# Optimization experiments

Hardware: AMD Instinct MI355X
Metric: run time of the kernel (lower is better)

Reference implementation:

```python
import jax, jax.numpy as jnp
import numpy as np

N_NODES = 50000
N_EDGES = 800000
HID = 128
HEADS = 1
VOCAB = 1001  # input_dim + 1
OUT = 16
NEG_SLOPE = 0.2  # DGL GATv2Conv default


def setup_inputs():
    key = jax.random.key(0)
    ks = jax.random.split(key, 12)
    s = 1.0 / np.sqrt(HID)
    inp = {}
    inp['feats'] = jax.random.randint(ks[0], (N_NODES, 2), 0, VOCAB, dtype=jnp.int64)
    inp['src'] = jax.random.randint(ks[1], (N_EDGES,), 0, N_NODES, dtype=jnp.int32)
    inp['dst'] = jax.random.randint(ks[2], (N_EDGES,), 0, N_NODES, dtype=jnp.int32)
    inp['key_emb'] = jax.random.normal(ks[3], (VOCAB, HID), jnp.float32)
    inp['val_emb'] = jax.random.normal(ks[4], (VOCAB, HID), jnp.float32)
    inp['W1'] = jax.random.uniform(ks[5], (HID, HEADS * HID), jnp.float32, -s, s)
    inp['attn1'] = jax.random.uniform(ks[6], (HEADS, HID), jnp.float32, -s, s)
    inp['W2'] = jax.random.uniform(ks[7], (HID, HEADS * HID), jnp.float32, -s, s)
    inp['attn2'] = jax.random.uniform(ks[8], (HEADS, HID), jnp.float32, -s, s)
    inp['cls_w'] = jax.random.uniform(ks[9], (HID, OUT), jnp.float32, -s, s)
    return inp


def _gatv2_layer(h, W, attn, src, dst):
    # share_weights=True: one linear transform for both src and dst roles
    feat = (h @ W).reshape(N_NODES, HEADS, HID)          # [N,H,D]
    e = jax.nn.leaky_relu(feat[src] + feat[dst], NEG_SLOPE)  # [E,H,D]
    logits = jnp.einsum('ehd,hd->eh', e, attn)            # [E,H]
    # segment softmax over incoming edges of each dst node
    m = jax.ops.segment_max(logits, dst, num_segments=N_NODES)  # [N,H]
    ex = jnp.exp(logits - m[dst])
    denom = jax.ops.segment_sum(ex, dst, num_segments=N_NODES)
    a = ex / denom[dst]                                   # [E,H]
    # weighted scatter-aggregate of src features to dst nodes
    return jax.ops.segment_sum(a[:, :, None] * feat[src], dst, num_segments=N_NODES)  # [N,H,D]


def reference(feats, src, dst, key_emb, val_emb, W1, attn1, W2, attn2, cls_w):
    h = jax.nn.relu(key_emb[feats[:, 0]] + val_emb[feats[:, 1]])  # [N,HID]
    h = _gatv2_layer(h, W1, attn1, src, dst).mean(axis=1)         # mean over heads
    h = _gatv2_layer(h, W2, attn2, src, dst).mean(axis=1)
    return h @ cls_w  # [N,OUT]
```

## Files before the change

### kernel.cpp

```cpp
#include <hip/hip_runtime.h>
#include <hip/hip_fp16.h>
#include <math.h>

#define HID 128

typedef _Float16 half8 __attribute__((ext_vector_type(8)));
typedef float floatx4 __attribute__((ext_vector_type(4)));

struct h4pack { __half2 a, b; };

__device__ __forceinline__ float4 h4tof4(h4pack h) {
  float2 lo = __half22float2(h.a);
  float2 hi = __half22float2(h.b);
  return make_float4(lo.x, lo.y, hi.x, hi.y);
}

__device__ __forceinline__ h4pack f4toh4(float4 v) {
  h4pack h;
  h.a = __floats2half2_rn(v.x, v.y);
  h.b = __floats2half2_rn(v.z, v.w);
  return h;
}

__global__ __launch_bounds__(256) void zero_kernel(int4* __restrict__ p, int n4) {
  int i = blockIdx.x * 256 + threadIdx.x;
  if (i < n4) p[i] = make_int4(0, 0, 0, 0);
}

__global__ __launch_bounds__(256) void hist_kernel(
    const int* __restrict__ dst, int* __restrict__ counts,
    int* __restrict__ rank, int E) {
  int e = blockIdx.x * 256 + threadIdx.x;
  if (e < E) rank[e] = atomicAdd(&counts[dst[e]], 1);
}

__global__ __launch_bounds__(256) void partial_kernel(
    const int* __restrict__ counts, int* __restrict__ partials, int N) {
  __shared__ int s[256];
  int idx = blockIdx.x * 256 + threadIdx.x;
  int c = (idx < N) ? counts[idx] : 0;
  s[threadIdx.x] = (idx < N) ? ((c + 7) & ~7) : 0;
  __syncthreads();
  for (int o = 128; o > 0; o >>= 1) {
    if (threadIdx.x < o) s[threadIdx.x] += s[threadIdx.x + o];
    __syncthreads();
  }
  if (threadIdx.x == 0) partials[blockIdx.x] = s[0];
}

__global__ __launch_bounds__(256) void scan2_kernel(
    const int* __restrict__ partials, int* __restrict__ bases, int NB) {
  __shared__ int s[256];
  int t = threadIdx.x;
  int v0 = (t < NB) ? partials[t] : 0;
  s[t] = v0;
  __syncthreads();
  for (int o = 1; o < 256; o <<= 1) {
    int v = (t >= o) ? s[t - o] : 0;
    __syncthreads();
    s[t] += v;
    __syncthreads();
  }
  bases[t] = s[t] - v0;
}

__global__ __launch_bounds__(256) void offs_kernel(
    const int* __restrict__ counts, const int* __restrict__ bases,
    int* __restrict__ offs, int* __restrict__ csr, int N) {
  __shared__ int s[256];
  int t = threadIdx.x;
  int idx = blockIdx.x * 256 + t;
  int deg = (idx < N) ? counts[idx] : 0;
  int c = (idx < N) ? ((deg + 7) & ~7) : 0;
  s[t] = c;
  __syncthreads();
  for (int o = 1; o < 256; o <<= 1) {
    int v = (t >= o) ? s[t - o] : 0;
    __syncthreads();
    s[t] += v;
    __syncthreads();
  }
  int base = bases[blockIdx.x];
  if (idx < N) {
    int o = base + s[t] - c;
    offs[idx] = o;
    for (int k = deg; k < c; ++k) csr[o + k] = 0;
  }
  if (idx == N - 1) offs[N] = base + s[t];
}

__global__ __launch_bounds__(256) void scatter_kernel(
    const int* __restrict__ src, const int* __restrict__ dst,
    const int* __restrict__ offs, const int* __restrict__ rank,
    int* __restrict__ csr, int E) {
  int e = blockIdx.x * 256 + threadIdx.x;
  if (e >= E) return;
  csr[offs[dst[e]] + rank[e]] = src[e];
}

__global__ __launch_bounds__(256) void embed_kernel(
    const int* __restrict__ feats, const float* __restrict__ ke,
    const float* __restrict__ ve, __half* __restrict__ h0, int N) {
  int gid = blockIdx.x * 256 + threadIdx.x;
  int n = gid >> 4, j = gid & 15;
  if (n >= N) return;
  int f0 = feats[2 * n], f1 = feats[2 * n + 1];
  const float4* a4 = (const float4*)(ke + (size_t)f0 * HID) + j * 2;
  const float4* b4 = (const float4*)(ve + (size_t)f1 * HID) + j * 2;
  float4 a0 = a4[0], a1 = a4[1], b0 = b4[0], b1 = b4[1];
  float4 v0, v1;
  v0.x = fmaxf(a0.x + b0.x, 0.f); v0.y = fmaxf(a0.y + b0.y, 0.f);
  v0.z = fmaxf(a0.z + b0.z, 0.f); v0.w = fmaxf(a0.w + b0.w, 0.f);
  v1.x = fmaxf(a1.x + b1.x, 0.f); v1.y = fmaxf(a1.y + b1.y, 0.f);
  v1.z = fmaxf(a1.z + b1.z, 0.f); v1.w = fmaxf(a1.w + b1.w, 0.f);
  h4pack* out = (h4pack*)h0 + (size_t)n * 32 + j * 2;
  out[0] = f4toh4(v0);
  out[1] = f4toh4(v1);
}

__global__ __launch_bounds__(256) void wprep_kernel(
    const float* __restrict__ W, __half* __restrict__ Wt) {
  int t = blockIdx.x * 256 + threadIdx.x;
  int k = t >> 7, c = t & 127;
  Wt[(size_t)c * HID + k] = __float2half(W[t]);
}

__global__ __launch_bounds__(256) void gemm_mfma_kernel(
    const __half* __restrict__ A, const __half* __restrict__ Wt,
    __half* __restrict__ F, int N) {
  int w = threadIdx.x >> 6;
  int lane = threadIdx.x & 63;
  int r = lane & 15, g = lane >> 4;
  int row0 = blockIdx.x * 64 + w * 16;
  if (row0 >= N) return;
  int arow = row0 + r;
  if (arow >= N) arow = N - 1;
  const half8* Ap = (const half8*)(A + (size_t)arow * HID + g * 8);
  half8 a0 = Ap[0];
  half8 a1 = Ap[4];
  half8 a2 = Ap[8];
  half8 a3 = Ap[12];
#pragma unroll
  for (int ct = 0; ct < 8; ++ct) {
    const half8* Bp = (const half8*)(Wt + (size_t)(ct * 16 + r) * HID + g * 8);
    half8 b0 = Bp[0], b1 = Bp[4], b2 = Bp[8], b3 = Bp[12];
    floatx4 c = {0.f, 0.f, 0.f, 0.f};
    c = __builtin_amdgcn_mfma_f32_16x16x32_f16(a0, b0, c, 0, 0, 0);
    c = __builtin_amdgcn_mfma_f32_16x16x32_f16(a1, b1, c, 0, 0, 0);
    c = __builtin_amdgcn_mfma_f32_16x16x32_f16(a2, b2, c, 0, 0, 0);
    c = __builtin_amdgcn_mfma_f32_16x16x32_f16(a3, b3, c, 0, 0, 0);
    int col = ct * 16 + r;
#pragma unroll
    for (int reg = 0; reg < 4; ++reg) {
      int row = row0 + g * 4 + reg;
      if (row < N) F[(size_t)row * HID + col] = __float2half(c[reg]);
    }
  }
}

__device__ __forceinline__ float dot4f(const float4& f, const float4& fd,
                                       const float4& a6, const float4& a4) {
  float t, p;
  t = f.x + fd.x; p = a6.x * t;         p = fmaf(a4.x, fabsf(t), p);
  t = f.y + fd.y; p = fmaf(a6.y, t, p); p = fmaf(a4.y, fabsf(t), p);
  t = f.z + fd.z; p = fmaf(a6.z, t, p); p = fmaf(a4.z, fabsf(t), p);
  t = f.w + fd.w; p = fmaf(a6.w, t, p); p = fmaf(a4.w, fabsf(t), p);
  return p;
}

__global__ __launch_bounds__(256) void gat_kernel(
    const __half* __restrict__ F, const int* __restrict__ offs,
    const int* __restrict__ counts, const int* __restrict__ csr,
    const float* __restrict__ attn, __half* __restrict__ Hout, int N) {
  int q = threadIdx.x & 31;
  int lane = threadIdx.x & 63;
  const h4pack* F4h = (const h4pack*)F;
  float4 av = ((const float4*)attn)[q];
  float4 a6, a4;
  a6.x = 0.6f * av.x; a6.y = 0.6f * av.y; a6.z = 0.6f * av.z; a6.w = 0.6f * av.w;
  a4.x = 0.4f * av.x; a4.y = 0.4f * av.y; a4.z = 0.4f * av.z; a4.w = 0.4f * av.w;
  int ib = (lane & 32) << 2;
  bool b1 = (q & 1) != 0;
  bool b2 = (q & 2) != 0;
  bool b4 = (q & 4) != 0;
  int stride = gridDim.x * 8;

  for (int node = blockIdx.x * 8 + (threadIdx.x >> 5); node < N; node += stride) {
    float4 fd = h4tof4(F4h[(size_t)node * 32 + q]);
    int beg = offs[node];
    int cnt = counts[node];
    float l = 0.f;
    float4 acc = make_float4(0.f, 0.f, 0.f, 0.f);

    int nit = (cnt + 7) >> 3;
    const int* cp = csr + beg;
    for (int it = 0; it < nit; ++it) {
      const int4* qp = (const int4*)(cp + 8 * it);
      int4 sa = qp[0];
      int4 sb = qp[1];
      float4 fa0 = h4tof4(F4h[(size_t)sa.x * 32 + q]);
      float4 fa1 = h4tof4(F4h[(size_t)sa.y * 32 + q]);
      float4 fa2 = h4tof4(F4h[(size_t)sa.z * 32 + q]);
      float4 fa3 = h4tof4(F4h[(size_t)sa.w * 32 + q]);
      float4 fb0 = h4tof4(F4h[(size_t)sb.x * 32 + q]);
      float4 fb1 = h4tof4(F4h[(size_t)sb.y * 32 + q]);
      float4 fb2 = h4tof4(F4h[(size_t)sb.z * 32 + q]);
      float4 fb3 = h4tof4(F4h[(size_t)sb.w * 32 + q]);
      int rem = cnt - 8 * it;
      float p0 = dot4f(fa0, fd, a6, a4);
      float p1 = (1 < rem) ? dot4f(fa1, fd, a6, a4) : -INFINITY;
      float p2 = (2 < rem) ? dot4f(fa2, fd, a6, a4) : -INFINITY;
      float p3 = (3 < rem) ? dot4f(fa3, fd, a6, a4) : -INFINITY;
      float p4 = (4 < rem) ? dot4f(fb0, fd, a6, a4) : -INFINITY;
      float p5 = (5 < rem) ? dot4f(fb1, fd, a6, a4) : -INFINITY;
      float p6 = (6 < rem) ? dot4f(fb2, fd, a6, a4) : -INFINITY;
      float p7 = (7 < rem) ? dot4f(fb3, fd, a6, a4) : -INFINITY;
      float u0 = p0 + __shfl_xor(p0, 1, 64);
      float u1 = p1 + __shfl_xor(p1, 1, 64);
      float u2 = p2 + __shfl_xor(p2, 1, 64);
      float u3 = p3 + __shfl_xor(p3, 1, 64);
      float u4 = p4 + __shfl_xor(p4, 1, 64);
      float u5 = p5 + __shfl_xor(p5, 1, 64);
      float u6 = p6 + __shfl_xor(p6, 1, 64);
      float u7 = p7 + __shfl_xor(p7, 1, 64);
      float c0 = b1 ? u1 : u0;
      float c1 = b1 ? u3 : u2;
      float c2 = b1 ? u5 : u4;
      float c3 = b1 ? u7 : u6;
      float d0 = c0 + __shfl_xor(c0, 2, 64);
      float d1 = c1 + __shfl_xor(c1, 2, 64);
      float d2 = c2 + __shfl_xor(c2, 2, 64);
      float d3 = c3 + __shfl_xor(c3, 2, 64);
      float w0 = b2 ? d1 : d0;
      float w1 = b2 ? d3 : d2;
      float x0 = w0 + __shfl_xor(w0, 4, 64);
      float x1 = w1 + __shfl_xor(w1, 4, 64);
      float r = b4 ? x1 : x0;
      r += __shfl_xor(r, 8, 64);
      r += __shfl_xor(r, 16, 64);
      float ex = __expf(r);
      int exi = __float_as_int(ex);
      float e0 = __int_as_float(__builtin_amdgcn_ds_bpermute(ib +  0, exi));
      float e1 = __int_as_float(__builtin_amdgcn_ds_bpermute(ib +  4, exi));
      float e2 = __int_as_float(__builtin_amdgcn_ds_bpermute(ib +  8, exi));
      float e3 = __int_as_float(__builtin_amdgcn_ds_bpermute(ib + 12, exi));
      float e4 = __int_as_float(__builtin_amdgcn_ds_bpermute(ib + 16, exi));
      float e5 = __int_as_float(__builtin_amdgcn_ds_bpermute(ib + 20, exi));
      float e6 = __int_as_float(__builtin_amdgcn_ds_bpermute(ib + 24, exi));
      float e7 = __int_as_float(__builtin_amdgcn_ds_bpermute(ib + 28, exi));
      l += ((e0 + e1) + (e2 + e3)) + ((e4 + e5) + (e6 + e7));
      acc.x = fmaf(e0, fa0.x, acc.x); acc.x = fmaf(e1, fa1.x, acc.x);
      acc.x = fmaf(e2, fa2.x, acc.x); acc.x = fmaf(e3, fa3.x, acc.x);
      acc.x = fmaf(e4, fb0.x, acc.x); acc.x = fmaf(e5, fb1.x, acc.x);
      acc.x = fmaf(e6, fb2.x, acc.x); acc.x = fmaf(e7, fb3.x, acc.x);
      acc.y = fmaf(e0, fa0.y, acc.y); acc.y = fmaf(e1, fa1.y, acc.y);
      acc.y = fmaf(e2, fa2.y, acc.y); acc.y = fmaf(e3, fa3.y, acc.y);
      acc.y = fmaf(e4, fb0.y, acc.y); acc.y = fmaf(e5, fb1.y, acc.y);
      acc.y = fmaf(e6, fb2.y, acc.y); acc.y = fmaf(e7, fb3.y, acc.y);
      acc.z = fmaf(e0, fa0.z, acc.z); acc.z = fmaf(e1, fa1.z, acc.z);
      acc.z = fmaf(e2, fa2.z, acc.z); acc.z = fmaf(e3, fa3.z, acc.z);
      acc.z = fmaf(e4, fb0.z, acc.z); acc.z = fmaf(e5, fb1.z, acc.z);
      acc.z = fmaf(e6, fb2.z, acc.z); acc.z = fmaf(e7, fb3.z, acc.z);
      acc.w = fmaf(e0, fa0.w, acc.w); acc.w = fmaf(e1, fa1.w, acc.w);
      acc.w = fmaf(e2, fa2.w, acc.w); acc.w = fmaf(e3, fa3.w, acc.w);
      acc.w = fmaf(e4, fb0.w, acc.w); acc.w = fmaf(e5, fb1.w, acc.w);
      acc.w = fmaf(e6, fb2.w, acc.w); acc.w = fmaf(e7, fb3.w, acc.w);
    }
    float inv = (l > 0.f) ? 1.f / l : 0.f;
    acc.x *= inv; acc.y *= inv; acc.z *= inv; acc.w *= inv;
    ((h4pack*)Hout)[(size_t)node * 32 + q] = f4toh4(acc);
  }
}

__global__ __launch_bounds__(256) void classify_kernel(
    const __half* __restrict__ H, const float* __restrict__ Wc,
    float* __restrict__ out, int N) {
  __shared__ float sW[HID * 16];
  __shared__ float sH[16][132];
  for (int i = threadIdx.x; i < HID * 16; i += 256) sW[i] = Wc[i];
  int row0 = blockIdx.x * 16;
  for (int i = threadIdx.x; i < 16 * 32; i += 256) {
    int r = i >> 5, j = i & 31;
    int row = row0 + r;
    float4 v = make_float4(0.f, 0.f, 0.f, 0.f);
    if (row < N) v = h4tof4(((const h4pack*)H)[(size_t)row * 32 + j]);
    ((float4*)&sH[r][0])[j] = v;
  }
  __syncthreads();
  int r = threadIdx.x >> 4;
  int c = threadIdx.x & 15;
  float acc = 0.f;
#pragma unroll 8
  for (int k = 0; k < HID; ++k) acc = fmaf(sH[r][k], sW[k * 16 + c], acc);
  int row = row0 + r;
  if (row < N) out[(size_t)row * 16 + c] = acc;
}

extern "C" void kernel_launch(void* const* d_in, const int* in_sizes, int n_in,
                              void* d_out, int out_size, void* d_ws, size_t ws_size,
                              hipStream_t stream) {
  const int* feats     = (const int*)d_in[0];
  const int* src       = (const int*)d_in[1];
  const int* dst       = (const int*)d_in[2];
  const float* key_emb = (const float*)d_in[3];
  const float* val_emb = (const float*)d_in[4];
  const float* W1      = (const float*)d_in[5];
  const float* attn1   = (const float*)d_in[6];
  const float* W2      = (const float*)d_in[7];
  const float* attn2   = (const float*)d_in[8];
  const float* cls_w   = (const float*)d_in[9];

  int N = in_sizes[0] / 2;
  int E = in_sizes[1];
  int NB = (N + 255) / 256;

  int Np = (N + 3) & ~3;
  int Ep = (E + 3) & ~3;
  char* ws = (char*)d_ws;
  __half* fbuf  = (__half*)ws;
  __half* hbuf  = (__half*)(ws + (size_t)Np * HID * 2);
  __half* ebuf  = (__half*)(ws + (size_t)Np * HID * 4);
  __half* Wt1   = (__half*)(ws + (size_t)Np * HID * 6);
  __half* Wt2   = Wt1 + HID * HID;
  int* counts   = (int*)(Wt2 + HID * HID);
  int* offs     = counts + Np;
  int* rank     = offs + Np + 4;
  int* csr      = rank + Ep;
  int* partials = csr + Ep + 8 * (size_t)Np;
  int* bases    = partials + 256;

  zero_kernel<<<(Np / 4 + 255) / 256, 256, 0, stream>>>((int4*)counts, Np / 4);

  hist_kernel<<<(E + 255) / 256, 256, 0, stream>>>(dst, counts, rank, E);
  partial_kernel<<<NB, 256, 0, stream>>>(counts, partials, N);
  scan2_kernel<<<1, 256, 0, stream>>>(partials, bases, NB);
  offs_kernel<<<NB, 256, 0, stream>>>(counts, bases, offs, csr, N);
  scatter_kernel<<<(E + 255) / 256, 256, 0, stream>>>(src, dst, offs, rank, csr, E);

  wprep_kernel<<<64, 256, 0, stream>>>(W1, Wt1);
  wprep_kernel<<<64, 256, 0, stream>>>(W2, Wt2);
  embed_kernel<<<((size_t)N * 16 + 255) / 256, 256, 0, stream>>>(
      feats, key_emb, val_emb, ebuf, N);

  int gblocks = (N + 63) / 64;
  int gatblocks = 2048;
  gemm_mfma_kernel<<<gblocks, 256, 0, stream>>>(ebuf, Wt1, fbuf, N);
  gat_kernel<<<gatblocks, 256, 0, stream>>>(
      fbuf, offs, counts, csr, attn1, hbuf, N);
  gemm_mfma_kernel<<<gblocks, 256, 0, stream>>>(hbuf, Wt2, fbuf, N);
  gat_kernel<<<gatblocks, 256, 0, stream>>>(
      fbuf, offs, counts, csr, attn2, hbuf, N);

  classify_kernel<<<(N + 15) / 16, 256, 0, stream>>>(hbuf, cls_w, (float*)d_out, N);
}
```

Before: 217.7 us.

## Use 16 lanes per node with 16-byte feature loads in GAT aggregation

The GAT kernel now gives each destination node 16 lanes instead of 32, with each lane loading 8 halves (16 bytes) per neighbor. This halves the lanes per gather and doubles the bytes per load. The grid-stride loop is replaced by one node per 16-lane group and a grid sized to the node count. The attention dot product accumulates signed and absolute parts separately and combines them at the end, and the reduction drops one shuffle stage. More registers per lane may lower occupancy, and a 16-lane group gathers fewer neighbors in parallel per node.

```diff
diff --git a/kernel.cpp b/kernel.cpp
--- a/kernel.cpp
+++ b/kernel.cpp
@@ -20,6 +20,12 @@
   h.a = __floats2half2_rn(v.x, v.y);
   h.b = __floats2half2_rn(v.z, v.w);
   return h;
+}
+
+__device__ __forceinline__ void cvt8(uint4 r, float4& lo, float4& hi) {
+  const h4pack* hp = (const h4pack*)&r;
+  lo = h4tof4(hp[0]);
+  hi = h4tof4(hp[1]);
 }
 
 __global__ __launch_bounds__(256) void zero_kernel(int4* __restrict__ p, int n4) {
@@ -158,118 +164,120 @@
   }
 }
 
-__device__ __forceinline__ float dot4f(const float4& f, const float4& fd,
-                                       const float4& a6, const float4& a4) {
-  float t, p;
-  t = f.x + fd.x; p = a6.x * t;         p = fmaf(a4.x, fabsf(t), p);
-  t = f.y + fd.y; p = fmaf(a6.y, t, p); p = fmaf(a4.y, fabsf(t), p);
-  t = f.z + fd.z; p = fmaf(a6.z, t, p); p = fmaf(a4.z, fabsf(t), p);
-  t = f.w + fd.w; p = fmaf(a6.w, t, p); p = fmaf(a4.w, fabsf(t), p);
-  return p;
+__device__ __forceinline__ float dot8f(uint4 raw, const float4& fd0, const float4& fd1,
+                                       const float4& av0, const float4& av1) {
+  float4 lo, hi;
+  cvt8(raw, lo, hi);
+  float t, pa = 0.f, pb = 0.f;
+  t = lo.x + fd0.x; pa = fmaf(av0.x, t, pa); pb = fmaf(av0.x, fabsf(t), pb);
+  t = lo.y + fd0.y; pa = fmaf(av0.y, t, pa); pb = fmaf(av0.y, fabsf(t), pb);
+  t = lo.z + fd0.z; pa = fmaf(av0.z, t, pa); pb = fmaf(av0.z, fabsf(t), pb);
+  t = lo.w + fd0.w; pa = fmaf(av0.w, t, pa); pb = fmaf(av0.w, fabsf(t), pb);
+  t = hi.x + fd1.x; pa = fmaf(av1.x, t, pa); pb = fmaf(av1.x, fabsf(t), pb);
+  t = hi.y + fd1.y; pa = fmaf(av1.y, t, pa); pb = fmaf(av1.y, fabsf(t), pb);
+  t = hi.z + fd1.z; pa = fmaf(av1.z, t, pa); pb = fmaf(av1.z, fabsf(t), pb);
+  t = hi.w + fd1.w; pa = fmaf(av1.w, t, pa); pb = fmaf(av1.w, fabsf(t), pb);
+  return 0.6f * pa + 0.4f * pb;
 }
 
 __global__ __launch_bounds__(256) void gat_kernel(
     const __half* __restrict__ F, const int* __restrict__ offs,
     const int* __restrict__ counts, const int* __restrict__ csr,
     const float* __restrict__ attn, __half* __restrict__ Hout, int N) {
-  int q = threadIdx.x & 31;
+  int node = blockIdx.x * 16 + (threadIdx.x >> 4);
+  if (node >= N) return;
+  int q = threadIdx.x & 15;
   int lane = threadIdx.x & 63;
-  const h4pack* F4h = (const h4pack*)F;
-  float4 av = ((const float4*)attn)[q];
-  float4 a6, a4;
-  a6.x = 0.6f * av.x; a6.y = 0.6f * av.y; a6.z = 0.6f * av.z; a6.w = 0.6f * av.w;
-  a4.x = 0.4f * av.x; a4.y = 0.4f * av.y; a4.z = 0.4f * av.z; a4.w = 0.4f * av.w;
-  int ib = (lane & 32) << 2;
+  const uint4* F16 = (const uint4*)F;
+  float4 fd0, fd1;
+  cvt8(F16[(size_t)node * 16 + q], fd0, fd1);
+  float4 av0 = ((const float4*)attn)[q * 2];
+  float4 av1 = ((const float4*)attn)[q * 2 + 1];
+  int ib = (lane & 48) << 2;
   bool b1 = (q & 1) != 0;
   bool b2 = (q & 2) != 0;
   bool b4 = (q & 4) != 0;
-  int stride = gridDim.x * 8;
-
-  for (int node = blockIdx.x * 8 + (threadIdx.x >> 5); node < N; node += stride) {
-    float4 fd = h4tof4(F4h[(size_t)node * 32 + q]);
-    int beg = offs[node];
-    int cnt = counts[node];
-    float l = 0.f;
-    float4 acc = make_float4(0.f, 0.f, 0.f, 0.f);
-
-    int nit = (cnt + 7) >> 3;
-    const int* cp = csr + beg;
-    for (int it = 0; it < nit; ++it) {
-      const int4* qp = (const int4*)(cp + 8 * it);
-      int4 sa = qp[0];
-      int4 sb = qp[1];
-      float4 fa0 = h4tof4(F4h[(size_t)sa.x * 32 + q]);
-      float4 fa1 = h4tof4(F4h[(size_t)sa.y * 32 + q]);
-      float4 fa2 = h4tof4(F4h[(size_t)sa.z * 32 + q]);
-      float4 fa3 = h4tof4(F4h[(size_t)sa.w * 32 + q]);
-      float4 fb0 = h4tof4(F4h[(size_t)sb.x * 32 + q]);
-      float4 fb1 = h4tof4(F4h[(size_t)sb.y * 32 + q]);
-      float4 fb2 = h4tof4(F4h[(size_t)sb.z * 32 + q]);
-      float4 fb3 = h4tof4(F4h[(size_t)sb.w * 32 + q]);
-      int rem = cnt - 8 * it;
-      float p0 = dot4f(fa0, fd, a6, a4);
-      float p1 = (1 < rem) ? dot4f(fa1, fd, a6, a4) : -INFINITY;
-      float p2 = (2 < rem) ? dot4f(fa2, fd, a6, a4) : -INFINITY;
-      float p3 = (3 < rem) ? dot4f(fa3, fd, a6, a4) : -INFINITY;
-      float p4 = (4 < rem) ? dot4f(fb0, fd, a6, a4) : -INFINITY;
-      float p5 = (5 < rem) ? dot4f(fb1, fd, a6, a4) : -INFINITY;
-      float p6 = (6 < rem) ? dot4f(fb2, fd, a6, a4) : -INFINITY;
-      float p7 = (7 < rem) ? dot4f(fb3, fd, a6, a4) : -INFINITY;
-      float u0 = p0 + __shfl_xor(p0, 1, 64);
-      float u1 = p1 + __shfl_xor(p1, 1, 64);
-      float u2 = p2 + __shfl_xor(p2, 1, 64);
-      float u3 = p3 + __shfl_xor(p3, 1, 64);
-      float u4 = p4 + __shfl_xor(p4, 1, 64);
-      float u5 = p5 + __shfl_xor(p5, 1, 64);
-      float u6 = p6 + __shfl_xor(p6, 1, 64);
-      float u7 = p7 + __shfl_xor(p7, 1, 64);
-      float c0 = b1 ? u1 : u0;
-      float c1 = b1 ? u3 : u2;
-      float c2 = b1 ? u5 : u4;
-      float c3 = b1 ? u7 : u6;
-      float d0 = c0 + __shfl_xor(c0, 2, 64);
-      float d1 = c1 + __shfl_xor(c1, 2, 64);
-      float d2 = c2 + __shfl_xor(c2, 2, 64);
-      float d3 = c3 + __shfl_xor(c3, 2, 64);
-      float w0 = b2 ? d1 : d0;
-      float w1 = b2 ? d3 : d2;
-      float x0 = w0 + __shfl_xor(w0, 4, 64);
-      float x1 = w1 + __shfl_xor(w1, 4, 64);
-      float r = b4 ? x1 : x0;
-      r += __shfl_xor(r, 8, 64);
-      r += __shfl_xor(r, 16, 64);
-      float ex = __expf(r);
-      int exi = __float_as_int(ex);
-      float e0 = __int_as_float(__builtin_amdgcn_ds_bpermute(ib +  0, exi));
-      float e1 = __int_as_float(__builtin_amdgcn_ds_bpermute(ib +  4, exi));
-      float e2 = __int_as_float(__builtin_amdgcn_ds_bpermute(ib +  8, exi));
-      float e3 = __int_as_float(__builtin_amdgcn_ds_bpermute(ib + 12, exi));
-      float e4 = __int_as_float(__builtin_amdgcn_ds_bpermute(ib + 16, exi));
-      float e5 = __int_as_float(__builtin_amdgcn_ds_bpermute(ib + 20, exi));
-      float e6 = __int_as_float(__builtin_amdgcn_ds_bpermute(ib + 24, exi));
-      float e7 = __int_as_float(__builtin_amdgcn_ds_bpermute(ib + 28, exi));
-      l += ((e0 + e1) + (e2 + e3)) + ((e4 + e5) + (e6 + e7));
-      acc.x = fmaf(e0, fa0.x, acc.x); acc.x = fmaf(e1, fa1.x, acc.x);
-      acc.x = fmaf(e2, fa2.x, acc.x); acc.x = fmaf(e3, fa3.x, acc.x);
-      acc.x = fmaf(e4, fb0.x, acc.x); acc.x = fmaf(e5, fb1.x, acc.x);
-      acc.x = fmaf(e6, fb2.x, acc.x); acc.x = fmaf(e7, fb3.x, acc.x);
-      acc.y = fmaf(e0, fa0.y, acc.y); acc.y = fmaf(e1, fa1.y, acc.y);
-      acc.y = fmaf(e2, fa2.y, acc.y); acc.y = fmaf(e3, fa3.y, acc.y);
-      acc.y = fmaf(e4, fb0.y, acc.y); acc.y = fmaf(e5, fb1.y, acc.y);
-      acc.y = fmaf(e6, fb2.y, acc.y); acc.y = fmaf(e7, fb3.y, acc.y);
-      acc.z = fmaf(e0, fa0.z, acc.z); acc.z = fmaf(e1, fa1.z, acc.z);
-      acc.z = fmaf(e2, fa2.z, acc.z); acc.z = fmaf(e3, fa3.z, acc.z);
-      acc.z = fmaf(e4, fb0.z, acc.z); acc.z = fmaf(e5, fb1.z, acc.z);
-      acc.z = fmaf(e6, fb2.z, acc.z); acc.z = fmaf(e7, fb3.z, acc.z);
-      acc.w = fmaf(e0, fa0.w, acc.w); acc.w = fmaf(e1, fa1.w, acc.w);
-      acc.w = fmaf(e2, fa2.w, acc.w); acc.w = fmaf(e3, fa3.w, acc.w);
-      acc.w = fmaf(e4, fb0.w, acc.w); acc.w = fmaf(e5, fb1.w, acc.w);
-      acc.w = fmaf(e6, fb2.w, acc.w); acc.w = fmaf(e7, fb3.w, acc.w);
-    }
-    float inv = (l > 0.f) ? 1.f / l : 0.f;
-    acc.x *= inv; acc.y *= inv; acc.z *= inv; acc.w *= inv;
-    ((h4pack*)Hout)[(size_t)node * 32 + q] = f4toh4(acc);
-  }
+
+  int beg = offs[node];
+  int cnt = counts[node];
+  float l = 0.f;
+  float4 acc0 = make_float4(0.f, 0.f, 0.f, 0.f), acc1 = acc0;
+
+  int nit = (cnt + 7) >> 3;
+  const int* cp = csr + beg;
+  for (int it = 0; it < nit; ++it) {
+    const int4* qp = (const int4*)(cp + 8 * it);
+    int4 sa = qp[0];
+    int4 sb = qp[1];
+    uint4 r0 = F16[(size_t)sa.x * 16 + q];
+    uint4 r1 = F16[(size_t)sa.y * 16 + q];
+    uint4 r2 = F16[(size_t)sa.z * 16 + q];
+    uint4 r3 = F16[(size_t)sa.w * 16 + q];
+    uint4 r4 = F16[(size_t)sb.x * 16 + q];
+    uint4 r5 = F16[(size_t)sb.y * 16 + q];
+    uint4 r6 = F16[(size_t)sb.z * 16 + q];
+    uint4 r7 = F16[(size_t)sb.w * 16 + q];
+    int rem = cnt - 8 * it;
+    float p0 = dot8f(r0, fd0, fd1, av0, av1);
+    float p1 = (1 < rem) ? dot8f(r1, fd0, fd1, av0, av1) : -INFINITY;
+    float p2 = (2 < rem) ? dot8f(r2, fd0, fd1, av0, av1) : -INFINITY;
+    float p3 = (3 < rem) ? dot8f(r3, fd0, fd1, av0, av1) : -INFINITY;
+    float p4 = (4 < rem) ? dot8f(r4, fd0, fd1, av0, av1) : -INFINITY;
+    float p5 = (5 < rem) ? dot8f(r5, fd0, fd1, av0, av1) : -INFINITY;
+    float p6 = (6 < rem) ? dot8f(r6, fd0, fd1, av0, av1) : -INFINITY;
+    float p7 = (7 < rem) ? dot8f(r7, fd0, fd1, av0, av1) : -INFINITY;
+    float u0 = p0 + __shfl_xor(p0, 1, 64);
+    float u1 = p1 + __shfl_xor(p1, 1, 64);
+    float u2 = p2 + __shfl_xor(p2, 1, 64);
+    float u3 = p3 + __shfl_xor(p3, 1, 64);
+    float u4 = p4 + __shfl_xor(p4, 1, 64);
+    float u5 = p5 + __shfl_xor(p5, 1, 64);
+    float u6 = p6 + __shfl_xor(p6, 1, 64);
+    float u7 = p7 + __shfl_xor(p7, 1, 64);
+    float c0 = b1 ? u1 : u0;
+    float c1 = b1 ? u3 : u2;
+    float c2 = b1 ? u5 : u4;
+    float c3 = b1 ? u7 : u6;
+    float d0 = c0 + __shfl_xor(c0, 2, 64);
+    float d1 = c1 + __shfl_xor(c1, 2, 64);
+    float d2 = c2 + __shfl_xor(c2, 2, 64);
+    float d3 = c3 + __shfl_xor(c3, 2, 64);
+    float e0s = b2 ? d1 : d0;
+    float e1s = b2 ? d3 : d2;
+    float f0s = e0s + __shfl_xor(e0s, 4, 64);
+    float f1s = e1s + __shfl_xor(e1s, 4, 64);
+    float g = b4 ? f1s : f0s;
+    float r = g + __shfl_xor(g, 8, 64);
+    float ex = __expf(r);
+    int exi = __float_as_int(ex);
+    float e0 = __int_as_float(__builtin_amdgcn_ds_bpermute(ib +  0, exi));
+    float e1 = __int_as_float(__builtin_amdgcn_ds_bpermute(ib +  4, exi));
+    float e2 = __int_as_float(__builtin_amdgcn_ds_bpermute(ib +  8, exi));
+    float e3 = __int_as_float(__builtin_amdgcn_ds_bpermute(ib + 12, exi));
+    float e4 = __int_as_float(__builtin_amdgcn_ds_bpermute(ib + 16, exi));
+    float e5 = __int_as_float(__builtin_amdgcn_ds_bpermute(ib + 20, exi));
+    float e6 = __int_as_float(__builtin_amdgcn_ds_bpermute(ib + 24, exi));
+    float e7 = __int_as_float(__builtin_amdgcn_ds_bpermute(ib + 28, exi));
+    l += ((e0 + e1) + (e2 + e3)) + ((e4 + e5) + (e6 + e7));
+    float4 lo, hi;
+#define ACC_EDGE(RAW, EV)                                                      \
+    cvt8(RAW, lo, hi);                                                         \
+    acc0.x = fmaf(EV, lo.x, acc0.x); acc0.y = fmaf(EV, lo.y, acc0.y);          \
+    acc0.z = fmaf(EV, lo.z, acc0.z); acc0.w = fmaf(EV, lo.w, acc0.w);          \
+    acc1.x = fmaf(EV, hi.x, acc1.x); acc1.y = fmaf(EV, hi.y, acc1.y);          \
+    acc1.z = fmaf(EV, hi.z, acc1.z); acc1.w = fmaf(EV, hi.w, acc1.w);
+    ACC_EDGE(r0, e0) ACC_EDGE(r1, e1) ACC_EDGE(r2, e2) ACC_EDGE(r3, e3)
+    ACC_EDGE(r4, e4) ACC_EDGE(r5, e5) ACC_EDGE(r6, e6) ACC_EDGE(r7, e7)
+#undef ACC_EDGE
+  }
+  float inv = (l > 0.f) ? 1.f / l : 0.f;
+  acc0.x *= inv; acc0.y *= inv; acc0.z *= inv; acc0.w *= inv;
+  acc1.x *= inv; acc1.y *= inv; acc1.z *= inv; acc1.w *= inv;
+  h4pack o0 = f4toh4(acc0), o1 = f4toh4(acc1);
+  uint4 ov;
+  h4pack* op = (h4pack*)&ov;
+  op[0] = o0; op[1] = o1;
+  ((uint4*)Hout)[(size_t)node * 16 + q] = ov;
 }
 
 __global__ __launch_bounds__(256) void classify_kernel(
@@ -343,7 +351,7 @@
       feats, key_emb, val_emb, ebuf, N);
 
   int gblocks = (N + 63) / 64;
-  int gatblocks = 2048;
+  int gatblocks = (N + 15) / 16;
   gemm_mfma_kernel<<<gblocks, 256, 0, stream>>>(ebuf, Wt1, fbuf, N);
   gat_kernel<<<gatblocks, 256, 0, stream>>>(
       fbuf, offs, counts, csr, attn1, hbuf, N);
```

Result: faster. 211.7 us (-2.7%).
